# Optimization experiments

Measured on AMD Instinct MI355X. Metric: run time of the kernel, lower is better.

Reference implementation:

```python
import jax, jax.numpy as jnp
import numpy as np

CLIP_VALUE = 5.0  # matches init clip_value


def setup_inputs() -> dict:
    B, T, I, H = 256, 400, 256, 512
    key = jax.random.key(0)
    k_x, k_ih, k_hh = jax.random.split(key, 3)
    scale = 1.0 / np.sqrt(I + H)  # is_encoder=True -> scale_dim = input+hidden
    x = jax.random.normal(k_x, (B, T, I), dtype=jnp.float32)
    h0 = jnp.zeros((B, H), dtype=jnp.float32)
    weight_ih = jax.random.normal(k_ih, (3 * H, I), dtype=jnp.float32) * scale
    weight_hh = jax.random.normal(k_hh, (3 * H, H), dtype=jnp.float32) * scale
    # bias_ih: ones, with the last H entries (new-gate bias) zeroed
    bias_ih = jnp.concatenate([jnp.ones(2 * H, jnp.float32), jnp.zeros(H, jnp.float32)])
    bias_hh = jnp.zeros(3 * H, dtype=jnp.float32)  # frozen zeros in the original
    return {"x": x, "h0": h0, "weight_ih": weight_ih, "bias_ih": bias_ih,
            "weight_hh": weight_hh, "bias_hh": bias_hh}


def reference(x, h0, weight_ih, bias_ih, weight_hh, bias_hh):
    H = h0.shape[-1]
    W_zr = weight_hh[:2 * H]          # [2H, H]
    W_n = weight_hh[2 * H:]           # [H, H]
    b_zr = bias_hh[:2 * H]
    b_n = bias_hh[2 * H:]
    # Precompute all input projections in one big GEMM: [B, T, 3H]
    x_all = jnp.einsum('bti,gi->btg', x, weight_ih) + bias_ih
    x_all_t = jnp.transpose(x_all, (1, 0, 2))  # time-major [T, B, 3H]

    def step(h, x_t):
        x_z, x_r, x_n = jnp.split(x_t, 3, axis=-1)
        h_zr = h @ W_zr.T + b_zr
        h_z, h_r = jnp.split(h_zr, 2, axis=-1)
        z = jax.nn.sigmoid(x_z + h_z)
        r = jax.nn.sigmoid(x_r + h_r)
        # NOTE: faithful to source precedence: (r * hidden) @ W_n^T + b_n
        h_n = (r * h) @ W_n.T + b_n
        n = jnp.tanh(x_n + h_n)
        h_new = z * h + (1.0 - z) * n
        h_new = jnp.clip(h_new, -CLIP_VALUE, CLIP_VALUE)
        return h_new, h_new

    h_last, out_t = jax.lax.scan(step, h0, x_all_t)
    output = jnp.transpose(out_t, (1, 0, 2))  # [B, T, H]
    return output, h_last
```

## Files before the change

### kernel.cpp

```cpp
#include <hip/hip_runtime.h>
#include <stdint.h>

#define B_DIM 256
#define T_DIM 400
#define I_DIMM 256
#define H_DIM 512
#define KH 512
#define KX 256
#define KU 768
#define MT 32
#define ACOLS 32
#define BCOLS 16
#define LDK 776

#define LDS_USHORTS (2*ACOLS*LDK + 2*BCOLS*LDK)
#define LDS_BYTES   (LDS_USHORTS*2 + 512*4)

#define OFF_FLAGA 0
#define OFF_FLAGB 2048
#define OFF_HFRAG 4096
#define FRAG_BYTES (16*16*64*32)
#define OFF_RHFRAG (OFF_HFRAG + FRAG_BYTES)
#define OFF_ZBUF   (OFF_RHFRAG + FRAG_BYTES)
#define OFF_XFRAG  (OFF_ZBUF + B_DIM*H_DIM*4)
#define XFRAG_BYTES ((size_t)T_DIM*16*8*2048)
#define WS_NEED    ((size_t)OFF_XFRAG + XFRAG_BYTES)

typedef __attribute__((ext_vector_type(8))) short short8v;
typedef __attribute__((ext_vector_type(4))) float f32x4;
typedef __attribute__((ext_vector_type(2))) unsigned long long u64x2;

__device__ __forceinline__ unsigned short f2bf(float f){
  unsigned u = __builtin_bit_cast(unsigned, f);
  unsigned r = (u + 0x7fffu + ((u >> 16) & 1u)) >> 16;
  return (unsigned short)r;
}
__device__ __forceinline__ float bf2f(unsigned short u){
  return __builtin_bit_cast(float, ((unsigned)u) << 16);
}
__device__ __forceinline__ f32x4 mfma16(short8v a, short8v b, f32x4 c){
  return __builtin_amdgcn_mfma_f32_16x16x32_bf16(a, b, c, 0, 0, 0);
}

__device__ __forceinline__ unsigned long long ld64_cg(const void* p){
  return __hip_atomic_load((const unsigned long long*)p, __ATOMIC_RELAXED,
                           __HIP_MEMORY_SCOPE_AGENT);
}
__device__ __forceinline__ unsigned short ld16_cg(const void* p){
  return __hip_atomic_load((const unsigned short*)p, __ATOMIC_RELAXED,
                           __HIP_MEMORY_SCOPE_AGENT);
}
__device__ __forceinline__ float ldf_cg(const float* p){
  return __hip_atomic_load(p, __ATOMIC_RELAXED, __HIP_MEMORY_SCOPE_AGENT);
}
__device__ __forceinline__ void st16_cg(void* p, unsigned v){
  asm volatile("global_store_short %0, %1, off sc0 sc1" :: "v"(p), "v"(v) : "memory");
}
__device__ __forceinline__ void stf_cg(float* p, float v){
  asm volatile("global_store_dword %0, %1, off sc0 sc1" :: "v"(p), "v"(v) : "memory");
}
#define VMCNT0() asm volatile("s_waitcnt vmcnt(0)" ::: "memory")

__device__ __forceinline__ void spin_ge(const unsigned* f, unsigned target){
  const unsigned* p = f + (threadIdx.x & 31);
  for (;;){
    unsigned v = __hip_atomic_load(p, __ATOMIC_RELAXED, __HIP_MEMORY_SCOPE_AGENT);
    if (__all((int)(v >= target))) break;
    __builtin_amdgcn_s_sleep(1);
  }
  asm volatile("" ::: "memory");
}

__device__ __forceinline__ size_t frag_off(int row, int col){
  int fragblk = (row >> 5)*2 + ((row >> 4) & 1);
  int kb   = col >> 5;
  int lane = (row & 15) + (((col & 31) >> 3) << 4);
  int e    = col & 7;
  return (size_t)fragblk*32768 + kb*2048 + lane*32 + e*2;
}

__global__ void gru_init(const float* __restrict__ h0, char* __restrict__ ws){
  unsigned* flags = (unsigned*)ws;
  char* hfrag = ws + OFF_HFRAG;
  int tid = blockIdx.x * blockDim.x + threadIdx.x;
  if (blockIdx.x == 0 && threadIdx.x < 1024) flags[threadIdx.x] = 0u;
  for (int idx = tid; idx < B_DIM*H_DIM; idx += gridDim.x * blockDim.x){
    float h = h0[idx];
    unsigned short hi = f2bf(h);
    unsigned short lo = f2bf(h - bf2f(hi));
    size_t off = frag_off(idx >> 9, idx & 511);
    *(unsigned short*)(hfrag + off)      = hi;
    *(unsigned short*)(hfrag + off + 16) = lo;
  }
}

__global__ void x_transcode(const float* __restrict__ x, char* __restrict__ xfrag){
  int gtid = blockIdx.x * blockDim.x + threadIdx.x;
  int w = gtid >> 6, lane = gtid & 63;
  if (w >= T_DIM*16*8) return;
  int t = w >> 7, rem = w & 127, rb = rem >> 3, kb = rem & 7;
  int row = rb*16 + (lane & 15);
  int kq  = (lane >> 4) * 8;
  const float* src = x + ((size_t)row*T_DIM + t)*I_DIMM + kb*32 + kq;
  f32x4 v0 = *(const f32x4*)src;
  f32x4 v1 = *(const f32x4*)(src + 4);
  short8v hi, lo;
  #pragma unroll
  for (int e = 0; e < 4; ++e){
    unsigned short h0b = f2bf(v0[e]), h1b = f2bf(v1[e]);
    hi[e] = (short)h0b;  hi[e+4] = (short)h1b;
    lo[e]   = (short)f2bf(v0[e] - bf2f(h0b));
    lo[e+4] = (short)f2bf(v1[e] - bf2f(h1b));
  }
  char* dst = xfrag + ((size_t)(t*16 + rb)*8 + kb)*2048 + lane*32;
  *(short8v*)dst = hi;
  *(short8v*)(dst + 16) = lo;
}

template<int XF>
__global__ void __launch_bounds__(256, 1) gru_scan(
    const float* __restrict__ x, const float* __restrict__ w_ih,
    const float* __restrict__ b_ih, const float* __restrict__ w_hh,
    const float* __restrict__ b_hh, const float* __restrict__ h0,
    float* __restrict__ out, char* __restrict__ ws)
{
  extern __shared__ unsigned short lds[];
  unsigned short* WAh = lds;
  unsigned short* WAl = WAh + ACOLS*LDK;
  unsigned short* WBh = WAl + ACOLS*LDK;
  unsigned short* WBl = WBh + BCOLS*LDK;
  float* red = (float*)(WBl + BCOLS*LDK);

  unsigned* flagsA = (unsigned*)(ws + OFF_FLAGA);
  unsigned* flagsB = (unsigned*)(ws + OFF_FLAGB);
  char* hfrag  = ws + OFF_HFRAG;
  char* rhfrag = ws + OFF_RHFRAG;
  float* zbuf  = (float*)(ws + OFF_ZBUF);
  const char* xfrag = ws + OFF_XFRAG;

  const int bid = blockIdx.x;
  const int it  = bid & 7;
  const int j   = bid >> 3;
  const int tid = threadIdx.x;
  const int lane = tid & 63;
  const int wv   = tid >> 6;
  unsigned* flagA = flagsA + it*32;
  unsigned* flagB = flagsB + it*32;

  for (int c = 0; c < ACOLS; ++c){
    int g = ACOLS*j + c;
    for (int k = tid; k < KU; k += 256){
      float w = (k < KH) ? w_hh[(size_t)g*KH + k] : w_ih[(size_t)g*KX + (k - KH)];
      unsigned short hi = f2bf(w);
      WAh[c*LDK + k] = hi;
      WAl[c*LDK + k] = f2bf(w - bf2f(hi));
    }
  }
  for (int c = 0; c < BCOLS; ++c){
    int g = 1024 + BCOLS*j + c;
    for (int k = tid; k < KU; k += 256){
      float w = (k < KH) ? w_hh[(size_t)g*KH + k] : w_ih[(size_t)g*KX + (k - KH)];
      unsigned short hi = f2bf(w);
      WBh[c*LDK + k] = hi;
      WBl[c*LDK + k] = f2bf(w - bf2f(hi));
    }
  }
  __syncthreads();

  const int l16 = lane & 15;
  const int lq  = lane >> 4;
  const int kq  = lq * 8;
  const int rowblk  = wv & 1;
  const int colblkA = wv >> 1;
  const int khalf   = wv >> 1;

  const int fragblk = it*2 + rowblk;
  const char* hA_base  = hfrag  + (size_t)fragblk*32768 + lane*32;
  const char* rhB_base = rhfrag + (size_t)fragblk*32768 + lane*32;
  const int arow = it*MT + rowblk*16 + l16;
  const size_t xrow_off = (size_t)arow * (T_DIM*I_DIMM);
  const int ldsA = (colblkA*16 + l16) * LDK;
  const int ldsB = l16 * LDK;

  const int zr = ACOLS*j + colblkA*16 + l16;
  const float biasA = b_ih[zr] + b_hh[zr];
  const int nc = BCOLS*j + l16;
  const float biasB = b_ih[1024 + nc] + b_hh[1024 + nc];
  const int mrow0 = it*MT + rowblk*16 + lq*4;

  const int hcs = zr & 511;
  size_t off_hv[4];
  #pragma unroll
  for (int r = 0; r < 4; ++r) off_hv[r] = frag_off(mrow0 + r, hcs);
  size_t off_hw[4];
  #pragma unroll
  for (int r = 0; r < 4; ++r) off_hw[r] = frag_off(mrow0 + r, nc);

  float h_reg[4];
  if (khalf == 0){
    #pragma unroll
    for (int r = 0; r < 4; ++r)
      h_reg[r] = h0[(size_t)(mrow0 + r)*H_DIM + nc];
  }

  unsigned long long hb0[4][4], hb1[4][4];

  auto LDH = [&](unsigned long long (&buf)[4][4], int c0){
    #pragma unroll
    for (int u = 0; u < 4; ++u){
      const char* p = hA_base + (size_t)(c0*4 + u)*2048;
      buf[u][0] = ld64_cg(p);      buf[u][1] = ld64_cg(p + 8);
      buf[u][2] = ld64_cg(p + 16); buf[u][3] = ld64_cg(p + 24);
    }
  };
  auto PRA = [&](unsigned long long (&buf)[4][4], int c0, f32x4& D){
    #pragma unroll
    for (int u = 0; u < 4; ++u){
      int k0 = (c0*4 + u)*32 + kq;
      u64x2 thi = {buf[u][0], buf[u][1]};
      u64x2 tlo = {buf[u][2], buf[u][3]};
      short8v ah = __builtin_bit_cast(short8v, thi);
      short8v al = __builtin_bit_cast(short8v, tlo);
      short8v bh = *(const short8v*)(WAh + ldsA + k0);
      short8v bl = *(const short8v*)(WAl + ldsA + k0);
      D = mfma16(ah, bh, D);
      D = mfma16(ah, bl, D);
      D = mfma16(al, bh, D);
    }
  };
  auto LDR = [&](unsigned long long (&buf)[4][4], int c0){
    #pragma unroll
    for (int u = 0; u < 4; ++u){
      const char* p = rhB_base + (size_t)((khalf*8) + c0*4 + u)*2048;
      buf[u][0] = ld64_cg(p);      buf[u][1] = ld64_cg(p + 8);
      buf[u][2] = ld64_cg(p + 16); buf[u][3] = ld64_cg(p + 24);
    }
  };
  auto PRB = [&](unsigned long long (&buf)[4][4], int c0, f32x4& D){
    #pragma unroll
    for (int u = 0; u < 4; ++u){
      int k0 = ((khalf*8) + c0*4 + u)*32 + kq;
      u64x2 thi = {buf[u][0], buf[u][1]};
      u64x2 tlo = {buf[u][2], buf[u][3]};
      short8v ah = __builtin_bit_cast(short8v, thi);
      short8v al = __builtin_bit_cast(short8v, tlo);
      short8v bh = *(const short8v*)(WBh + ldsB + k0);
      short8v bl = *(const short8v*)(WBl + ldsB + k0);
      D = mfma16(ah, bh, D);
      D = mfma16(ah, bl, D);
      D = mfma16(al, bh, D);
    }
  };
  auto XCONV = [&](const float* xp, short8v& ah, short8v& al){
    f32x4 v0 = *(const f32x4*)xp;
    f32x4 v1 = *(const f32x4*)(xp + 4);
    #pragma unroll
    for (int e = 0; e < 4; ++e){
      unsigned short h0b = f2bf(v0[e]), h1b = f2bf(v1[e]);
      ah[e] = (short)h0b;  ah[e+4] = (short)h1b;
      al[e]   = (short)f2bf(v0[e] - bf2f(h0b));
      al[e+4] = (short)f2bf(v1[e] - bf2f(h1b));
    }
  };

  for (int t = 0; t < T_DIM; ++t){
    const char* xf_base = xfrag + ((size_t)t*16 + fragblk)*8*2048 + lane*32;
    const float* xt = x + (size_t)t * I_DIMM;

    f32x4 D = {0.f, 0.f, 0.f, 0.f};
    #pragma unroll
    for (int kb = 0; kb < 8; ++kb){
      short8v ah, al;
      if (XF){
        const char* p = xf_base + kb*2048;
        ah = *(const short8v*)p;
        al = *(const short8v*)(p + 16);
      } else {
        XCONV(xt + xrow_off + kb*32 + kq, ah, al);
      }
      int k0 = KH + kb*32 + kq;
      short8v bh = *(const short8v*)(WAh + ldsA + k0);
      short8v bl = *(const short8v*)(WAl + ldsA + k0);
      D = mfma16(ah, bh, D);
      D = mfma16(ah, bl, D);
      D = mfma16(al, bh, D);
    }

    if (wv == 0) spin_ge(flagB, (unsigned)t);
    __syncthreads();

    unsigned short hvh[4], hvl[4];
    #pragma unroll
    for (int r = 0; r < 4; ++r){
      hvh[r] = ld16_cg(hfrag + off_hv[r]);
      hvl[r] = ld16_cg(hfrag + off_hv[r] + 16);
    }

    LDH(hb0, 0); LDH(hb1, 1);
    PRA(hb0, 0, D); LDH(hb0, 2);
    PRA(hb1, 1, D); LDH(hb1, 3);
    PRA(hb0, 2, D); PRA(hb1, 3, D);

    if (j < 16){
      #pragma unroll
      for (int r = 0; r < 4; ++r){
        float a = D[r] + biasA;
        float zv = 1.f / (1.f + __expf(-a));
        stf_cg(zbuf + (size_t)(mrow0 + r)*H_DIM + zr, zv);
      }
    } else {
      #pragma unroll
      for (int r = 0; r < 4; ++r){
        float a = D[r] + biasA;
        float rv = 1.f / (1.f + __expf(-a));
        float rh = rv * (bf2f(hvh[r]) + bf2f(hvl[r]));
        unsigned short hi = f2bf(rh);
        unsigned short lo = f2bf(rh - bf2f(hi));
        st16_cg(rhfrag + off_hv[r],      (unsigned)hi);
        st16_cg(rhfrag + off_hv[r] + 16, (unsigned)lo);
      }
    }
    VMCNT0();
    __syncthreads();
    if (tid == 0)
      __hip_atomic_store(&flagA[j], (unsigned)(t+1), __ATOMIC_RELAXED,
                         __HIP_MEMORY_SCOPE_AGENT);

    f32x4 Dn = {0.f, 0.f, 0.f, 0.f};
    #pragma unroll
    for (int u = 0; u < 4; ++u){
      int kb = khalf*4 + u;
      short8v ah, al;
      if (XF){
        const char* p = xf_base + kb*2048;
        ah = *(const short8v*)p;
        al = *(const short8v*)(p + 16);
      } else {
        XCONV(xt + xrow_off + kb*32 + kq, ah, al);
      }
      int k0 = KH + kb*32 + kq;
      short8v bh = *(const short8v*)(WBh + ldsB + k0);
      short8v bl = *(const short8v*)(WBl + ldsB + k0);
      Dn = mfma16(ah, bh, Dn);
      Dn = mfma16(ah, bl, Dn);
      Dn = mfma16(al, bh, Dn);
    }

    if (wv == 0) spin_ge(flagA, (unsigned)(t+1));
    __syncthreads();

    float zv[4];
    #pragma unroll
    for (int r = 0; r < 4; ++r)
      zv[r] = ldf_cg(zbuf + (size_t)(mrow0 + r)*H_DIM + nc);

    LDR(hb0, 0); LDR(hb1, 1);
    PRB(hb0, 0, Dn); PRB(hb1, 1, Dn);

    if (khalf == 1){
      #pragma unroll
      for (int r = 0; r < 4; ++r)
        red[rowblk*256 + (lq*4 + r)*16 + l16] = Dn[r];
    }
    __syncthreads();
    if (khalf == 0){
      #pragma unroll
      for (int r = 0; r < 4; ++r){
        float a = Dn[r] + red[rowblk*256 + (lq*4 + r)*16 + l16] + biasB;
        float ea = __expf(2.f * fabsf(a));
        float nv = 1.f - 2.f / (ea + 1.f);
        nv = (a < 0.f) ? -nv : nv;
        int row = mrow0 + r;
        float hn = zv[r]*h_reg[r] + (1.f - zv[r])*nv;
        hn = fminf(5.f, fmaxf(-5.f, hn));
        unsigned short hi = f2bf(hn);
        unsigned short lo = f2bf(hn - bf2f(hi));
        st16_cg(hfrag + off_hw[r],      (unsigned)hi);
        st16_cg(hfrag + off_hw[r] + 16, (unsigned)lo);
        out[(size_t)row*(T_DIM*H_DIM) + (size_t)t*H_DIM + nc] = hn;
        h_reg[r] = hn;
        if (t == T_DIM - 1)
          out[(size_t)B_DIM*T_DIM*H_DIM + (size_t)row*H_DIM + nc] = hn;
      }
    }
    VMCNT0();
    __syncthreads();
    if (tid == 0)
      __hip_atomic_store(&flagB[j], (unsigned)(t+1), __ATOMIC_RELAXED,
                         __HIP_MEMORY_SCOPE_AGENT);
  }
}

extern "C" void kernel_launch(void* const* d_in, const int* in_sizes, int n_in,
                              void* d_out, int out_size, void* d_ws, size_t ws_size,
                              hipStream_t stream){
  const float* x    = (const float*)d_in[0];
  const float* h0   = (const float*)d_in[1];
  const float* w_ih = (const float*)d_in[2];
  const float* b_ih = (const float*)d_in[3];
  const float* w_hh = (const float*)d_in[4];
  const float* b_hh = (const float*)d_in[5];
  float* out = (float*)d_out;
  char* ws = (char*)d_ws;

  gru_init<<<128, 256, 0, stream>>>(h0, ws);

  if (ws_size >= WS_NEED){
    x_transcode<<<(T_DIM*16*8*64 + 255)/256, 256, 0, stream>>>(x, ws + OFF_XFRAG);
    hipFuncSetAttribute((const void*)gru_scan<1>,
                        hipFuncAttributeMaxDynamicSharedMemorySize, LDS_BYTES);
    gru_scan<1><<<256, 256, LDS_BYTES, stream>>>(x, w_ih, b_ih, w_hh, b_hh, h0,
                                                 out, ws);
  } else {
    hipFuncSetAttribute((const void*)gru_scan<0>,
                        hipFuncAttributeMaxDynamicSharedMemorySize, LDS_BYTES);
    gru_scan<0><<<256, 256, LDS_BYTES, stream>>>(x, w_ih, b_ih, w_hh, b_hh, h0,
                                                 out, ws);
  }
}
```

Before: 4.748 ms.

## Vectorize cross-block h/rh/z exchanges via LDS transpose and drop block barrier spins

The per-element 16-bit hi/lo stores of rh and h into the fragment-layout global buffers are replaced by an LDS transpose. Each lane then writes one 128-bit coherent store per fragment row. The z buffer is re-laid out so each thread stores and loads four gate values as one 16-byte access. Flag spinning now runs in every wave with 64-bit flag loads instead of wave 0 spinning followed by __syncthreads, and the output stores are moved after the flag release so they leave the critical path. The intent is to cut global store count and synchronisation latency in the serial recurrence, at the cost of extra LDS traffic and more complex indexing.

```diff
diff --git a/kernel.cpp b/kernel.cpp
--- a/kernel.cpp
+++ b/kernel.cpp
@@ -14,11 +14,11 @@
 #define LDK 776
 
 #define LDS_USHORTS (2*ACOLS*LDK + 2*BCOLS*LDK)
-#define LDS_BYTES   (LDS_USHORTS*2 + 512*4)
+#define LDS_BYTES   (LDS_USHORTS*2 + (512 + 1280)*4)
 
 #define OFF_FLAGA 0
-#define OFF_FLAGB 2048
-#define OFF_HFRAG 4096
+#define OFF_FLAGB 1024
+#define OFF_HFRAG 8192
 #define FRAG_BYTES (16*16*64*32)
 #define OFF_RHFRAG (OFF_HFRAG + FRAG_BYTES)
 #define OFF_ZBUF   (OFF_RHFRAG + FRAG_BYTES)
@@ -26,14 +26,15 @@
 #define XFRAG_BYTES ((size_t)T_DIM*16*8*2048)
 #define WS_NEED    ((size_t)OFF_XFRAG + XFRAG_BYTES)
 
+typedef unsigned long long u64;
 typedef __attribute__((ext_vector_type(8))) short short8v;
 typedef __attribute__((ext_vector_type(4))) float f32x4;
-typedef __attribute__((ext_vector_type(2))) unsigned long long u64x2;
+typedef __attribute__((ext_vector_type(4))) unsigned uint4v;
+typedef __attribute__((ext_vector_type(2))) u64 u64x2;
 
 __device__ __forceinline__ unsigned short f2bf(float f){
   unsigned u = __builtin_bit_cast(unsigned, f);
-  unsigned r = (u + 0x7fffu + ((u >> 16) & 1u)) >> 16;
-  return (unsigned short)r;
+  return (unsigned short)((u + 0x7fffu + ((u >> 16) & 1u)) >> 16);
 }
 __device__ __forceinline__ float bf2f(unsigned short u){
   return __builtin_bit_cast(float, ((unsigned)u) << 16);
@@ -42,30 +43,24 @@
   return __builtin_amdgcn_mfma_f32_16x16x32_bf16(a, b, c, 0, 0, 0);
 }
 
-__device__ __forceinline__ unsigned long long ld64_cg(const void* p){
-  return __hip_atomic_load((const unsigned long long*)p, __ATOMIC_RELAXED,
-                           __HIP_MEMORY_SCOPE_AGENT);
-}
-__device__ __forceinline__ unsigned short ld16_cg(const void* p){
-  return __hip_atomic_load((const unsigned short*)p, __ATOMIC_RELAXED,
-                           __HIP_MEMORY_SCOPE_AGENT);
-}
-__device__ __forceinline__ float ldf_cg(const float* p){
-  return __hip_atomic_load(p, __ATOMIC_RELAXED, __HIP_MEMORY_SCOPE_AGENT);
-}
-__device__ __forceinline__ void st16_cg(void* p, unsigned v){
-  asm volatile("global_store_short %0, %1, off sc0 sc1" :: "v"(p), "v"(v) : "memory");
-}
-__device__ __forceinline__ void stf_cg(float* p, float v){
-  asm volatile("global_store_dword %0, %1, off sc0 sc1" :: "v"(p), "v"(v) : "memory");
+__device__ __forceinline__ u64 ld64_cg(const void* p){
+  return __hip_atomic_load((const u64*)p, __ATOMIC_RELAXED, __HIP_MEMORY_SCOPE_AGENT);
+}
+__device__ __forceinline__ unsigned ld16_cg(const void* p){
+  return (unsigned)__hip_atomic_load((const unsigned short*)p, __ATOMIC_RELAXED,
+                                     __HIP_MEMORY_SCOPE_AGENT);
+}
+__device__ __forceinline__ void cst128(void* p, uint4v v){
+  asm volatile("global_store_dwordx4 %0, %1, off sc0 sc1" :: "v"(p), "v"(v) : "memory");
 }
 #define VMCNT0() asm volatile("s_waitcnt vmcnt(0)" ::: "memory")
 
-__device__ __forceinline__ void spin_ge(const unsigned* f, unsigned target){
-  const unsigned* p = f + (threadIdx.x & 31);
+__device__ __forceinline__ void spin32(const unsigned* f, unsigned target){
+  const u64* p = (const u64*)(f + ((threadIdx.x & 15) << 1));
   for (;;){
-    unsigned v = __hip_atomic_load(p, __ATOMIC_RELAXED, __HIP_MEMORY_SCOPE_AGENT);
-    if (__all((int)(v >= target))) break;
+    u64 v = __hip_atomic_load(p, __ATOMIC_RELAXED, __HIP_MEMORY_SCOPE_AGENT);
+    bool ok = ((unsigned)v >= target) & ((unsigned)(v >> 32) >= target);
+    if (__all((int)ok)) break;
     __builtin_amdgcn_s_sleep(1);
   }
   asm volatile("" ::: "memory");
@@ -80,11 +75,10 @@
 }
 
 __global__ void gru_init(const float* __restrict__ h0, char* __restrict__ ws){
-  unsigned* flags = (unsigned*)ws;
+  int gtid = blockIdx.x * blockDim.x + threadIdx.x;
+  if (gtid < 2048) ((unsigned*)ws)[gtid] = 0u;
   char* hfrag = ws + OFF_HFRAG;
-  int tid = blockIdx.x * blockDim.x + threadIdx.x;
-  if (blockIdx.x == 0 && threadIdx.x < 1024) flags[threadIdx.x] = 0u;
-  for (int idx = tid; idx < B_DIM*H_DIM; idx += gridDim.x * blockDim.x){
+  for (int idx = gtid; idx < B_DIM*H_DIM; idx += gridDim.x * blockDim.x){
     float h = h0[idx];
     unsigned short hi = f2bf(h);
     unsigned short lo = f2bf(h - bf2f(hi));
@@ -129,10 +123,9 @@
   unsigned short* WAl = WAh + ACOLS*LDK;
   unsigned short* WBh = WAl + ACOLS*LDK;
   unsigned short* WBl = WBh + BCOLS*LDK;
-  float* red = (float*)(WBl + BCOLS*LDK);
-
-  unsigned* flagsA = (unsigned*)(ws + OFF_FLAGA);
-  unsigned* flagsB = (unsigned*)(ws + OFF_FLAGB);
+  float* red   = (float*)(WBl + BCOLS*LDK);
+  float* tpose = red + 512;
+
   char* hfrag  = ws + OFF_HFRAG;
   char* rhfrag = ws + OFF_RHFRAG;
   float* zbuf  = (float*)(ws + OFF_ZBUF);
@@ -144,8 +137,8 @@
   const int tid = threadIdx.x;
   const int lane = tid & 63;
   const int wv   = tid >> 6;
-  unsigned* flagA = flagsA + it*32;
-  unsigned* flagB = flagsB + it*32;
+  unsigned* flagsA = (unsigned*)(ws + OFF_FLAGA) + it*32;
+  unsigned* flagsB = (unsigned*)(ws + OFF_FLAGB) + it*32;
 
   for (int c = 0; c < ACOLS; ++c){
     int g = ACOLS*j + c;
@@ -192,20 +185,15 @@
   size_t off_hv[4];
   #pragma unroll
   for (int r = 0; r < 4; ++r) off_hv[r] = frag_off(mrow0 + r, hcs);
-  size_t off_hw[4];
-  #pragma unroll
-  for (int r = 0; r < 4; ++r) off_hw[r] = frag_off(mrow0 + r, nc);
-
-  float h_reg[4];
-  if (khalf == 0){
-    #pragma unroll
-    for (int r = 0; r < 4; ++r)
-      h_reg[r] = h0[(size_t)(mrow0 + r)*H_DIM + nc];
-  }
-
-  unsigned long long hb0[4][4], hb1[4][4];
-
-  auto LDH = [&](unsigned long long (&buf)[4][4], int c0){
+
+  float* zst = zbuf + ((size_t)it*512 + hcs)*32 + rowblk*16 + lq*4;
+  const float* zld = zbuf + ((size_t)it*512 + nc)*32 + rowblk*16 + lq*4;
+  char* rhkb = rhfrag + (size_t)fragblk*32768 + (size_t)((j - 16) & 15)*2048;
+  char* hkb  = hfrag  + (size_t)fragblk*32768 + (size_t)(j >> 1)*2048;
+
+  u64 hb0[4][4], hb1[4][4];
+
+  auto LDH = [&](u64 (&buf)[4][4], int c0){
     #pragma unroll
     for (int u = 0; u < 4; ++u){
       const char* p = hA_base + (size_t)(c0*4 + u)*2048;
@@ -213,7 +201,7 @@
       buf[u][2] = ld64_cg(p + 16); buf[u][3] = ld64_cg(p + 24);
     }
   };
-  auto PRA = [&](unsigned long long (&buf)[4][4], int c0, f32x4& D){
+  auto PRA = [&](u64 (&buf)[4][4], int c0, f32x4& D){
     #pragma unroll
     for (int u = 0; u < 4; ++u){
       int k0 = (c0*4 + u)*32 + kq;
@@ -223,12 +211,10 @@
       short8v al = __builtin_bit_cast(short8v, tlo);
       short8v bh = *(const short8v*)(WAh + ldsA + k0);
       short8v bl = *(const short8v*)(WAl + ldsA + k0);
-      D = mfma16(ah, bh, D);
-      D = mfma16(ah, bl, D);
-      D = mfma16(al, bh, D);
-    }
-  };
-  auto LDR = [&](unsigned long long (&buf)[4][4], int c0){
+      D = mfma16(ah, bh, D); D = mfma16(ah, bl, D); D = mfma16(al, bh, D);
+    }
+  };
+  auto LDR = [&](u64 (&buf)[4][4], int c0){
     #pragma unroll
     for (int u = 0; u < 4; ++u){
       const char* p = rhB_base + (size_t)((khalf*8) + c0*4 + u)*2048;
@@ -236,7 +222,7 @@
       buf[u][2] = ld64_cg(p + 16); buf[u][3] = ld64_cg(p + 24);
     }
   };
-  auto PRB = [&](unsigned long long (&buf)[4][4], int c0, f32x4& D){
+  auto PRB = [&](u64 (&buf)[4][4], int c0, f32x4& D){
     #pragma unroll
     for (int u = 0; u < 4; ++u){
       int k0 = ((khalf*8) + c0*4 + u)*32 + kq;
@@ -246,9 +232,7 @@
       short8v al = __builtin_bit_cast(short8v, tlo);
       short8v bh = *(const short8v*)(WBh + ldsB + k0);
       short8v bl = *(const short8v*)(WBl + ldsB + k0);
-      D = mfma16(ah, bh, D);
-      D = mfma16(ah, bl, D);
-      D = mfma16(al, bh, D);
+      D = mfma16(ah, bh, D); D = mfma16(ah, bl, D); D = mfma16(al, bh, D);
     }
   };
   auto XCONV = [&](const float* xp, short8v& ah, short8v& al){
@@ -262,6 +246,38 @@
       al[e+4] = (short)f2bf(v1[e] - bf2f(h1b));
     }
   };
+  auto TPOSE = [&](const float (&v)[4], char* fragkb, int colq_base){
+    float* tw = tpose + wv*320;
+    #pragma unroll
+    for (int r = 0; r < 4; ++r) tw[(lq*4 + r)*20 + l16] = v[r];
+    int b = (lane >> 4) & 1;
+    const float* tr = tpose + wv*320 + (lane & 15)*20 + b*8;
+    f32x4 w0 = *(const f32x4*)tr;
+    f32x4 w1 = *(const f32x4*)(tr + 4);
+    uint4v wd;
+    if (lane < 32){
+      unsigned h0b=f2bf(w0[0]), h1b=f2bf(w0[1]), h2b=f2bf(w0[2]), h3b=f2bf(w0[3]);
+      unsigned h4b=f2bf(w1[0]), h5b=f2bf(w1[1]), h6b=f2bf(w1[2]), h7b=f2bf(w1[3]);
+      wd.x = h0b | (h1b<<16); wd.y = h2b | (h3b<<16);
+      wd.z = h4b | (h5b<<16); wd.w = h6b | (h7b<<16);
+    } else {
+      unsigned l0=f2bf(w0[0]-bf2f(f2bf(w0[0]))), l1=f2bf(w0[1]-bf2f(f2bf(w0[1])));
+      unsigned l2=f2bf(w0[2]-bf2f(f2bf(w0[2]))), l3=f2bf(w0[3]-bf2f(f2bf(w0[3])));
+      unsigned l4=f2bf(w1[0]-bf2f(f2bf(w1[0]))), l5=f2bf(w1[1]-bf2f(f2bf(w1[1])));
+      unsigned l6=f2bf(w1[2]-bf2f(f2bf(w1[2]))), l7=f2bf(w1[3]-bf2f(f2bf(w1[3])));
+      wd.x = l0 | (l1<<16); wd.y = l2 | (l3<<16);
+      wd.z = l4 | (l5<<16); wd.w = l6 | (l7<<16);
+    }
+    int fl = (lane & 15) + (colq_base + b)*16;
+    cst128(fragkb + fl*32 + ((lane < 32) ? 0 : 16), wd);
+  };
+
+  float h_reg[4];
+  if (khalf == 0){
+    #pragma unroll
+    for (int r = 0; r < 4; ++r)
+      h_reg[r] = h0[(size_t)(mrow0 + r)*H_DIM + nc];
+  }
 
   for (int t = 0; t < T_DIM; ++t){
     const char* xf_base = xfrag + ((size_t)t*16 + fragblk)*8*2048 + lane*32;
@@ -281,49 +297,44 @@
       int k0 = KH + kb*32 + kq;
       short8v bh = *(const short8v*)(WAh + ldsA + k0);
       short8v bl = *(const short8v*)(WAl + ldsA + k0);
-      D = mfma16(ah, bh, D);
-      D = mfma16(ah, bl, D);
-      D = mfma16(al, bh, D);
-    }
-
-    if (wv == 0) spin_ge(flagB, (unsigned)t);
-    __syncthreads();
-
-    unsigned short hvh[4], hvl[4];
+      D = mfma16(ah, bh, D); D = mfma16(ah, bl, D); D = mfma16(al, bh, D);
+    }
+
+    spin32(flagsB, (unsigned)t);
+
+    unsigned hvh[4], hvl[4];
     #pragma unroll
     for (int r = 0; r < 4; ++r){
       hvh[r] = ld16_cg(hfrag + off_hv[r]);
       hvl[r] = ld16_cg(hfrag + off_hv[r] + 16);
     }
-
     LDH(hb0, 0); LDH(hb1, 1);
     PRA(hb0, 0, D); LDH(hb0, 2);
     PRA(hb1, 1, D); LDH(hb1, 3);
     PRA(hb0, 2, D); PRA(hb1, 3, D);
 
     if (j < 16){
+      f32x4 zq;
       #pragma unroll
       for (int r = 0; r < 4; ++r){
         float a = D[r] + biasA;
-        float zv = 1.f / (1.f + __expf(-a));
-        stf_cg(zbuf + (size_t)(mrow0 + r)*H_DIM + zr, zv);
-      }
+        zq[r] = 1.f / (1.f + __expf(-a));
+      }
+      cst128(zst, __builtin_bit_cast(uint4v, zq));
     } else {
+      float rhv[4];
       #pragma unroll
       for (int r = 0; r < 4; ++r){
         float a = D[r] + biasA;
         float rv = 1.f / (1.f + __expf(-a));
-        float rh = rv * (bf2f(hvh[r]) + bf2f(hvl[r]));
-        unsigned short hi = f2bf(rh);
-        unsigned short lo = f2bf(rh - bf2f(hi));
-        st16_cg(rhfrag + off_hv[r],      (unsigned)hi);
-        st16_cg(rhfrag + off_hv[r] + 16, (unsigned)lo);
-      }
+        rhv[r] = rv * (bf2f((unsigned short)hvh[r]) + bf2f((unsigned short)hvl[r]));
+      }
+      TPOSE(rhv, rhkb, colblkA*2);
     }
     VMCNT0();
     __syncthreads();
     if (tid == 0)
-      __hip_atomic_store(&flagA[j], (unsigned)(t+1), __ATOMIC_RELAXED,
+      __hip_atomic_store(flagsA + j, (unsigned)(t+1), __ATOMIC_RELAXED,
                          __HIP_MEMORY_SCOPE_AGENT);
 
     f32x4 Dn = {0.f, 0.f, 0.f, 0.f};
@@ -341,21 +352,20 @@
       int k0 = KH + kb*32 + kq;
       short8v bh = *(const short8v*)(WBh + ldsB + k0);
       short8v bl = *(const short8v*)(WBl + ldsB + k0);
-      Dn = mfma16(ah, bh, Dn);
-      Dn = mfma16(ah, bl, Dn);
-      Dn = mfma16(al, bh, Dn);
-    }
-
-    if (wv == 0) spin_ge(flagA, (unsigned)(t+1));
-    __syncthreads();
-
-    float zv[4];
-    #pragma unroll
-    for (int r = 0; r < 4; ++r)
-      zv[r] = ldf_cg(zbuf + (size_t)(mrow0 + r)*H_DIM + nc);
-
+      Dn = mfma16(ah, bh, Dn); Dn = mfma16(ah, bl, Dn); Dn = mfma16(al, bh, Dn);
+    }
+
+    spin32(flagsA, (unsigned)(t+1));
+
+    f32x4 zq = {0.f, 0.f, 0.f, 0.f};
+    if (khalf == 0){
+      u64 z0 = ld64_cg(zld), z1 = ld64_cg((const char*)zld + 8);
+      u64x2 zz = {z0, z1};
+      zq = __builtin_bit_cast(f32x4, zz);
+    }
     LDR(hb0, 0); LDR(hb1, 1);
-    PRB(hb0, 0, Dn); PRB(hb1, 1, Dn);
+    PRB(hb0, 0, Dn);
+    PRB(hb1, 1, Dn);
 
     if (khalf == 1){
       #pragma unroll
@@ -363,6 +373,7 @@
         red[rowblk*256 + (lq*4 + r)*16 + l16] = Dn[r];
     }
     __syncthreads();
+    float hn[4];
     if (khalf == 0){
       #pragma unroll
       for (int r = 0; r < 4; ++r){
@@ -370,24 +381,27 @@
         float ea = __expf(2.f * fabsf(a));
         float nv = 1.f - 2.f / (ea + 1.f);
         nv = (a < 0.f) ? -nv : nv;
-        int row = mrow0 + r;
-        float hn = zv[r]*h_reg[r] + (1.f - zv[r])*nv;
-        hn = fminf(5.f, fmaxf(-5.f, hn));
-        unsigned short hi = f2bf(hn);
-        unsigned short lo = f2bf(hn - bf2f(hi));
-        st16_cg(hfrag + off_hw[r],      (unsigned)hi);
-        st16_cg(hfrag + off_hw[r] + 16, (unsigned)lo);
-        out[(size_t)row*(T_DIM*H_DIM) + (size_t)t*H_DIM + nc] = hn;
-        h_reg[r] = hn;
-        if (t == T_DIM - 1)
-          out[(size_t)B_DIM*T_DIM*H_DIM + (size_t)row*H_DIM + nc] = hn;
-      }
+        float hnv = zq[r]*h_reg[r] + (1.f - zq[r])*nv;
+        hnv = fminf(5.f, fmaxf(-5.f, hnv));
+        hn[r] = hnv;
+        h_reg[r] = hnv;
+      }
+      TPOSE(hn, hkb, (j & 1)*2);
     }
     VMCNT0();
     __syncthreads();
     if (tid == 0)
-      __hip_atomic_store(&flagB[j], (unsigned)(t+1), __ATOMIC_RELAXED,
+      __hip_atomic_store(flagsB + j, (unsigned)(t+1), __ATOMIC_RELAXED,
                          __HIP_MEMORY_SCOPE_AGENT);
+    if (khalf == 0){
+      #pragma unroll
+      for (int r = 0; r < 4; ++r){
+        int row = mrow0 + r;
+        out[(size_t)row*(T_DIM*H_DIM) + (size_t)t*H_DIM + nc] = hn[r];
+        if (t == T_DIM - 1)
+          out[(size_t)B_DIM*T_DIM*H_DIM + (size_t)row*H_DIM + nc] = hn[r];
+      }
+    }
   }
 }
 
@@ -409,12 +423,10 @@
     x_transcode<<<(T_DIM*16*8*64 + 255)/256, 256, 0, stream>>>(x, ws + OFF_XFRAG);
     hipFuncSetAttribute((const void*)gru_scan<1>,
                         hipFuncAttributeMaxDynamicSharedMemorySize, LDS_BYTES);
-    gru_scan<1><<<256, 256, LDS_BYTES, stream>>>(x, w_ih, b_ih, w_hh, b_hh, h0,
-                                                 out, ws);
+    gru_scan<1><<<256, 256, LDS_BYTES, stream>>>(x, w_ih, b_ih, w_hh, b_hh, h0, out, ws);
   } else {
     hipFuncSetAttribute((const void*)gru_scan<0>,
                         hipFuncAttributeMaxDynamicSharedMemorySize, LDS_BYTES);
-    gru_scan<0><<<256, 256, LDS_BYTES, stream>>>(x, w_ih, b_ih, w_hh, b_hh, h0,
-                                                 out, ws);
-  }
-}
+    gru_scan<0><<<256, 256, LDS_BYTES, stream>>>(x, w_ih, b_ih, w_hh, b_hh, h0, out, ws);
+  }
+}
```

Measured after the change: 5.194 ms. 9.4% more time.

## Per-wave flag polling, prefetch flags, and defer output stores past signal

Applied to the files above, without the earlier changes.

Replaces the wave-0 spin plus __syncthreads barrier before each phase with a flag prefetch issued before the input MFMA loop and a per-wave check, so every wave spins on its own only if the producers are not yet done. The hvh/zbuf loads are restricted to the waves that use them, and the global output stores are moved after the flagB release so the critical-path signal is not delayed by the large output writes. This aims to shorten the per-timestep cross-block synchronization latency of the persistent scan. Removing the block barrier relies on per-wave visibility of the agent-scope loads being sufficient, which is a correctness risk.

```diff
diff --git a/kernel.cpp b/kernel.cpp
--- a/kernel.cpp
+++ b/kernel.cpp
@@ -26,14 +26,14 @@
 #define XFRAG_BYTES ((size_t)T_DIM*16*8*2048)
 #define WS_NEED    ((size_t)OFF_XFRAG + XFRAG_BYTES)
 
+typedef unsigned long long u64;
 typedef __attribute__((ext_vector_type(8))) short short8v;
 typedef __attribute__((ext_vector_type(4))) float f32x4;
-typedef __attribute__((ext_vector_type(2))) unsigned long long u64x2;
+typedef __attribute__((ext_vector_type(2))) u64 u64x2;
 
 __device__ __forceinline__ unsigned short f2bf(float f){
   unsigned u = __builtin_bit_cast(unsigned, f);
-  unsigned r = (u + 0x7fffu + ((u >> 16) & 1u)) >> 16;
-  return (unsigned short)r;
+  return (unsigned short)((u + 0x7fffu + ((u >> 16) & 1u)) >> 16);
 }
 __device__ __forceinline__ float bf2f(unsigned short u){
   return __builtin_bit_cast(float, ((unsigned)u) << 16);
@@ -42,13 +42,12 @@
   return __builtin_amdgcn_mfma_f32_16x16x32_bf16(a, b, c, 0, 0, 0);
 }
 
-__device__ __forceinline__ unsigned long long ld64_cg(const void* p){
-  return __hip_atomic_load((const unsigned long long*)p, __ATOMIC_RELAXED,
-                           __HIP_MEMORY_SCOPE_AGENT);
-}
-__device__ __forceinline__ unsigned short ld16_cg(const void* p){
-  return __hip_atomic_load((const unsigned short*)p, __ATOMIC_RELAXED,
-                           __HIP_MEMORY_SCOPE_AGENT);
+__device__ __forceinline__ u64 ld64_cg(const void* p){
+  return __hip_atomic_load((const u64*)p, __ATOMIC_RELAXED, __HIP_MEMORY_SCOPE_AGENT);
+}
+__device__ __forceinline__ unsigned ld16_cg(const void* p){
+  return (unsigned)__hip_atomic_load((const unsigned short*)p, __ATOMIC_RELAXED,
+                                     __HIP_MEMORY_SCOPE_AGENT);
 }
 __device__ __forceinline__ float ldf_cg(const float* p){
   return __hip_atomic_load(p, __ATOMIC_RELAXED, __HIP_MEMORY_SCOPE_AGENT);
@@ -196,16 +195,11 @@
   #pragma unroll
   for (int r = 0; r < 4; ++r) off_hw[r] = frag_off(mrow0 + r, nc);
 
-  float h_reg[4];
-  if (khalf == 0){
-    #pragma unroll
-    for (int r = 0; r < 4; ++r)
-      h_reg[r] = h0[(size_t)(mrow0 + r)*H_DIM + nc];
-  }
-
-  unsigned long long hb0[4][4], hb1[4][4];
-
-  auto LDH = [&](unsigned long long (&buf)[4][4], int c0){
+  char* rhkb = rhfrag + (size_t)fragblk*32768 + (size_t)((j - 16) & 15)*2048;
+
+  u64 hb0[4][4], hb1[4][4];
+
+  auto LDH = [&](u64 (&buf)[4][4], int c0){
     #pragma unroll
     for (int u = 0; u < 4; ++u){
       const char* p = hA_base + (size_t)(c0*4 + u)*2048;
@@ -213,7 +207,7 @@
       buf[u][2] = ld64_cg(p + 16); buf[u][3] = ld64_cg(p + 24);
     }
   };
-  auto PRA = [&](unsigned long long (&buf)[4][4], int c0, f32x4& D){
+  auto PRA = [&](u64 (&buf)[4][4], int c0, f32x4& D){
     #pragma unroll
     for (int u = 0; u < 4; ++u){
       int k0 = (c0*4 + u)*32 + kq;
@@ -223,12 +217,10 @@
       short8v al = __builtin_bit_cast(short8v, tlo);
       short8v bh = *(const short8v*)(WAh + ldsA + k0);
       short8v bl = *(const short8v*)(WAl + ldsA + k0);
-      D = mfma16(ah, bh, D);
-      D = mfma16(ah, bl, D);
-      D = mfma16(al, bh, D);
+      D = mfma16(ah, bh, D); D = mfma16(ah, bl, D); D = mfma16(al, bh, D);
     }
   };
-  auto LDR = [&](unsigned long long (&buf)[4][4], int c0){
+  auto LDR = [&](u64 (&buf)[4][4], int c0){
     #pragma unroll
     for (int u = 0; u < 4; ++u){
       const char* p = rhB_base + (size_t)((khalf*8) + c0*4 + u)*2048;
@@ -236,7 +228,7 @@
       buf[u][2] = ld64_cg(p + 16); buf[u][3] = ld64_cg(p + 24);
     }
   };
-  auto PRB = [&](unsigned long long (&buf)[4][4], int c0, f32x4& D){
+  auto PRB = [&](u64 (&buf)[4][4], int c0, f32x4& D){
     #pragma unroll
     for (int u = 0; u < 4; ++u){
       int k0 = ((khalf*8) + c0*4 + u)*32 + kq;
@@ -246,9 +238,7 @@
       short8v al = __builtin_bit_cast(short8v, tlo);
       short8v bh = *(const short8v*)(WBh + ldsB + k0);
       short8v bl = *(const short8v*)(WBl + ldsB + k0);
-      D = mfma16(ah, bh, D);
-      D = mfma16(ah, bl, D);
-      D = mfma16(al, bh, D);
+      D = mfma16(ah, bh, D); D = mfma16(ah, bl, D); D = mfma16(al, bh, D);
     }
   };
   auto XCONV = [&](const float* xp, short8v& ah, short8v& al){
@@ -263,10 +253,19 @@
     }
   };
 
+  float h_reg[4];
+  if (khalf == 0){
+    #pragma unroll
+    for (int r = 0; r < 4; ++r)
+      h_reg[r] = h0[(size_t)(mrow0 + r)*H_DIM + nc];
+  }
+
   for (int t = 0; t < T_DIM; ++t){
     const char* xf_base = xfrag + ((size_t)t*16 + fragblk)*8*2048 + lane*32;
     const float* xt = x + (size_t)t * I_DIMM;
 
+    unsigned pvA = __hip_atomic_load(flagB + (tid & 31), __ATOMIC_RELAXED,
+                                     __HIP_MEMORY_SCOPE_AGENT);
     f32x4 D = {0.f, 0.f, 0.f, 0.f};
     #pragma unroll
     for (int kb = 0; kb < 8; ++kb){
@@ -281,21 +280,20 @@
       int k0 = KH + kb*32 + kq;
       short8v bh = *(const short8v*)(WAh + ldsA + k0);
       short8v bl = *(const short8v*)(WAl + ldsA + k0);
-      D = mfma16(ah, bh, D);
-      D = mfma16(ah, bl, D);
-      D = mfma16(al, bh, D);
-    }
-
-    if (wv == 0) spin_ge(flagB, (unsigned)t);
-    __syncthreads();
-
-    unsigned short hvh[4], hvl[4];
-    #pragma unroll
-    for (int r = 0; r < 4; ++r){
-      hvh[r] = ld16_cg(hfrag + off_hv[r]);
-      hvl[r] = ld16_cg(hfrag + off_hv[r] + 16);
-    }
-
+      D = mfma16(ah, bh, D); D = mfma16(ah, bl, D); D = mfma16(al, bh, D);
+    }
+    if (!__all((int)(pvA >= (unsigned)t)))
+      spin_ge(flagB, (unsigned)t);
+    asm volatile("" ::: "memory");
+
+    unsigned hvh[4], hvl[4];
+    if (j >= 16){
+      #pragma unroll
+      for (int r = 0; r < 4; ++r){
+        hvh[r] = ld16_cg(hfrag + off_hv[r]);
+        hvl[r] = ld16_cg(hfrag + off_hv[r] + 16);
+      }
+    }
     LDH(hb0, 0); LDH(hb1, 1);
     PRA(hb0, 0, D); LDH(hb0, 2);
     PRA(hb1, 1, D); LDH(hb1, 3);
@@ -313,19 +311,22 @@
       for (int r = 0; r < 4; ++r){
         float a = D[r] + biasA;
         float rv = 1.f / (1.f + __expf(-a));
-        float rh = rv * (bf2f(hvh[r]) + bf2f(hvl[r]));
+        float rh = rv * (bf2f((unsigned short)hvh[r]) + bf2f((unsigned short)hvl[r]));
         unsigned short hi = f2bf(rh);
         unsigned short lo = f2bf(rh - bf2f(hi));
-        st16_cg(rhfrag + off_hv[r],      (unsigned)hi);
-        st16_cg(rhfrag + off_hv[r] + 16, (unsigned)lo);
+        size_t fo = off_hv[r] - ((size_t)fragblk*32768 + (size_t)((j-16)&15)*2048);
+        st16_cg(rhkb + fo,      (unsigned)hi);
+        st16_cg(rhkb + fo + 16, (unsigned)lo);
       }
     }
     VMCNT0();
     __syncthreads();
     if (tid == 0)
-      __hip_atomic_store(&flagA[j], (unsigned)(t+1), __ATOMIC_RELAXED,
+      __hip_atomic_store(flagA + j, (unsigned)(t+1), __ATOMIC_RELAXED,
                          __HIP_MEMORY_SCOPE_AGENT);
 
+    unsigned pvB = __hip_atomic_load(flagA + (tid & 31), __ATOMIC_RELAXED,
+                                     __HIP_MEMORY_SCOPE_AGENT);
     f32x4 Dn = {0.f, 0.f, 0.f, 0.f};
     #pragma unroll
     for (int u = 0; u < 4; ++u){
@@ -341,21 +342,21 @@
       int k0 = KH + kb*32 + kq;
       short8v bh = *(const short8v*)(WBh + ldsB + k0);
       short8v bl = *(const short8v*)(WBl + ldsB + k0);
-      Dn = mfma16(ah, bh, Dn);
-      Dn = mfma16(ah, bl, Dn);
-      Dn = mfma16(al, bh, Dn);
-    }
-
-    if (wv == 0) spin_ge(flagA, (unsigned)(t+1));
-    __syncthreads();
+      Dn = mfma16(ah, bh, Dn); Dn = mfma16(ah, bl, Dn); Dn = mfma16(al, bh, Dn);
+    }
+    if (!__all((int)(pvB >= (unsigned)(t+1))))
+      spin_ge(flagA, (unsigned)(t+1));
+    asm volatile("" ::: "memory");
 
     float zv[4];
-    #pragma unroll
-    for (int r = 0; r < 4; ++r)
-      zv[r] = ldf_cg(zbuf + (size_t)(mrow0 + r)*H_DIM + nc);
-
+    if (khalf == 0){
+      #pragma unroll
+      for (int r = 0; r < 4; ++r)
+        zv[r] = ldf_cg(zbuf + (size_t)(mrow0 + r)*H_DIM + nc);
+    }
     LDR(hb0, 0); LDR(hb1, 1);
-    PRB(hb0, 0, Dn); PRB(hb1, 1, Dn);
+    PRB(hb0, 0, Dn);
+    PRB(hb1, 1, Dn);
 
     if (khalf == 1){
       #pragma unroll
@@ -363,6 +364,7 @@
         red[rowblk*256 + (lq*4 + r)*16 + l16] = Dn[r];
     }
     __syncthreads();
+    float hn[4];
     if (khalf == 0){
       #pragma unroll
       for (int r = 0; r < 4; ++r){
@@ -370,24 +372,30 @@
         float ea = __expf(2.f * fabsf(a));
         float nv = 1.f - 2.f / (ea + 1.f);
         nv = (a < 0.f) ? -nv : nv;
-        int row = mrow0 + r;
-        float hn = zv[r]*h_reg[r] + (1.f - zv[r])*nv;
-        hn = fminf(5.f, fmaxf(-5.f, hn));
-        unsigned short hi = f2bf(hn);
-        unsigned short lo = f2bf(hn - bf2f(hi));
+        float hnv = zv[r]*h_reg[r] + (1.f - zv[r])*nv;
+        hnv = fminf(5.f, fmaxf(-5.f, hnv));
+        unsigned short hi = f2bf(hnv);
+        unsigned short lo = f2bf(hnv - bf2f(hi));
         st16_cg(hfrag + off_hw[r],      (unsigned)hi);
         st16_cg(hfrag + off_hw[r] + 16, (unsigned)lo);
-        out[(size_t)row*(T_DIM*H_DIM) + (size_t)t*H_DIM + nc] = hn;
-        h_reg[r] = hn;
-        if (t == T_DIM - 1)
-          out[(size_t)B_DIM*T_DIM*H_DIM + (size_t)row*H_DIM + nc] = hn;
+        h_reg[r] = hnv;
+        hn[r] = hnv;
       }
     }
     VMCNT0();
     __syncthreads();
     if (tid == 0)
-      __hip_atomic_store(&flagB[j], (unsigned)(t+1), __ATOMIC_RELAXED,
+      __hip_atomic_store(flagB + j, (unsigned)(t+1), __ATOMIC_RELAXED,
                          __HIP_MEMORY_SCOPE_AGENT);
+    if (khalf == 0){
+      #pragma unroll
+      for (int r = 0; r < 4; ++r){
+        int row = mrow0 + r;
+        out[(size_t)row*(T_DIM*H_DIM) + (size_t)t*H_DIM + nc] = hn[r];
+        if (t == T_DIM - 1)
+          out[(size_t)B_DIM*T_DIM*H_DIM + (size_t)row*H_DIM + nc] = hn[r];
+      }
+    }
   }
 }
 
@@ -409,12 +417,10 @@
     x_transcode<<<(T_DIM*16*8*64 + 255)/256, 256, 0, stream>>>(x, ws + OFF_XFRAG);
     hipFuncSetAttribute((const void*)gru_scan<1>,
                         hipFuncAttributeMaxDynamicSharedMemorySize, LDS_BYTES);
-    gru_scan<1><<<256, 256, LDS_BYTES, stream>>>(x, w_ih, b_ih, w_hh, b_hh, h0,
-                                                 out, ws);
+    gru_scan<1><<<256, 256, LDS_BYTES, stream>>>(x, w_ih, b_ih, w_hh, b_hh, h0, out, ws);
   } else {
     hipFuncSetAttribute((const void*)gru_scan<0>,
                         hipFuncAttributeMaxDynamicSharedMemorySize, LDS_BYTES);
-    gru_scan<0><<<256, 256, LDS_BYTES, stream>>>(x, w_ih, b_ih, w_hh, b_hh, h0,
-                                                 out, ws);
-  }
-}
+    gru_scan<0><<<256, 256, LDS_BYTES, stream>>>(x, w_ih, b_ih, w_hh, b_hh, h0, out, ws);
+  }
+}
```

Result: slower. 6.115 ms (+28.8%).
